# Optimization experiments

Hardware: AMD Instinct MI355X
Metric: run time of the kernel (lower is better)

Reference implementation:

```python
import jax, jax.numpy as jnp
import numpy as np

B = 65536
M = 16          # message_size
DEPTH = 6
WDL = 64
IN_DIM = 45 + 9 * M    # 9 mask + 4*9 board + 9*M messages
OUT_DIM = 9 * M


def setup_inputs() -> dict:
    key = jax.random.key(0)
    ks = jax.random.split(key, 8)
    input_mask = (jax.random.uniform(ks[0], (B, 9, 9)) < 0.5).astype(jnp.float32)
    input_board = (jax.random.uniform(ks[1], (B, 2, 10, 9)) < 0.5).astype(jnp.float32)
    # stacked per-om linears for every depth layer: [depth, 9, in, out]
    layer_w = jax.random.normal(ks[2], (DEPTH, 9, IN_DIM, OUT_DIM), jnp.float32) * (1.0 / np.sqrt(IN_DIM))
    layer_b = jnp.zeros((DEPTH, 9, OUT_DIM), jnp.float32)
    common_w = jax.random.normal(ks[3], (81 * M, 81 + WDL), jnp.float32) * (1.0 / np.sqrt(81 * M))
    common_b = jnp.zeros((81 + WDL,), jnp.float32)
    wdl_w = jax.random.normal(ks[4], (WDL, 3), jnp.float32) * (1.0 / np.sqrt(WDL))
    wdl_b = jnp.zeros((3,), jnp.float32)
    return {
        "input_mask": input_mask,
        "input_board": input_board,
        "layer_w": layer_w,
        "layer_b": layer_b,
        "common_w": common_w,
        "common_b": common_b,
        "wdl_w": wdl_w,
        "wdl_b": wdl_b,
    }


def reference(input_mask, input_board, layer_w, layer_b, common_w, common_b, wdl_w, wdl_b):
    b = input_mask.shape[0]
    m = layer_w.shape[-1] // 9
    depth = layer_w.shape[0]

    # per-om static features: mask[:,om], board[:,0,om], board[:,1,om], global cells
    g0 = jnp.broadcast_to(input_board[:, 0, 9:10, :], (b, 9, 9))
    g1 = jnp.broadcast_to(input_board[:, 1, 9:10, :], (b, 9, 9))
    static = jnp.concatenate(
        [input_mask, input_board[:, 0, :9, :], input_board[:, 1, :9, :], g0, g1],
        axis=-1,
    )  # [B, 9(om), 45]

    messages = jnp.zeros((b, 9, 9, m), input_mask.dtype)  # [B, src_om, dst_om, m]
    for d in range(depth):
        # messages[:, :, om, :] flattened -> gather along axis 2 for each om
        msg_in = messages.transpose(0, 2, 1, 3).reshape(b, 9, 9 * m)  # [B, om, 9m]
        x = jnp.concatenate([static, msg_in], axis=-1)  # [B, 9, 45+9m]
        # 9 distinct small linears, batched as one einsum
        h = jnp.einsum("boi,oij->boj", x, layer_w[d]) + layer_b[d]
        messages = jax.nn.relu(h).reshape(b, 9, 9, m)

    common = messages.reshape(b, 81 * m) @ common_w + common_b
    policy = common[:, :81]
    wdl_hidden = jax.nn.relu(common[:, 81:])
    wdl = wdl_hidden @ wdl_w + wdl_b
    return (wdl, policy)
```

## Files before the change

kernel.cpp:

```cpp
#include <hip/hip_runtime.h>
#include <hip/hip_bf16.h>
#include <stdint.h>


typedef __attribute__((ext_vector_type(4))) float    f32x4;
typedef __attribute__((ext_vector_type(4))) _Float16 f16x4;
typedef __attribute__((ext_vector_type(8))) _Float16 f16x8;
typedef unsigned long long u64;
typedef unsigned int u32;

#define STEP_BYTES 55296
#define PHA_SZ     30720
#define PHB_SZ     24576
#define CMN_STRIDE 41472
#define CSL_SZ     46080
#define CPA_SZ     23040
#define CPB_SZ     18432
#define WS_LAYER   (54*STEP_BYTES)
#define LDS_TOTAL  (2*PHA_SZ)

__device__ __forceinline__ unsigned short f2h(float f) {
  return __builtin_bit_cast(unsigned short, (_Float16)f);
}
__device__ __forceinline__ u64 as_u64(f16x4 v) { return __builtin_bit_cast(u64, v); }
__device__ __forceinline__ f16x4 as_f16x4(u64 v) { return __builtin_bit_cast(f16x4, v); }

__device__ __forceinline__ f32x4 mfma16(f16x4 a, f16x4 b, f32x4 c) {
#if __has_builtin(__builtin_amdgcn_mfma_f32_16x16x16f16)
  return __builtin_amdgcn_mfma_f32_16x16x16f16(a, b, c, 0, 0, 0);
#else
  asm("v_mfma_f32_16x16x16_f16 %0, %1, %2, %0" : "+v"(c) : "v"(a), "v"(b));
  return c;
#endif
}

__device__ __forceinline__ float static_feat(const float* __restrict__ mask,
                                             const float* __restrict__ board,
                                             int b, int o, int kidx) {
  if (kidx < 9)  return mask [b*81  + o*9 + kidx];
  if (kidx < 18) return board[b*180 +       o*9 + (kidx - 9)];
  if (kidx < 27) return board[b*180 + 90 +  o*9 + (kidx - 18)];
  if (kidx < 36) return board[b*180 +       81 + (kidx - 27)];
  if (kidx < 45) return board[b*180 + 90 +  81 + (kidx - 36)];
  return 0.f;
}

template<int NTH>
__device__ __forceinline__ void stage_n(const unsigned char* __restrict__ src,
                                        unsigned char* dstlds, int nbytes, int tid) {
  const int n16 = nbytes / 16;
  const int ubase = tid & ~63;
  for (int k = 0; k * NTH < n16; ++k) {
    const int idx = k * NTH + tid;
    if (idx < n16) {
      __builtin_amdgcn_global_load_lds(
          (const __attribute__((address_space(1))) void*)(src + (size_t)idx * 16),
          (__attribute__((address_space(3))) void*)(dstlds + (size_t)(k * NTH + ubase) * 16),
          16, 0, 0);
    }
  }
}


template<int P, int FIRST>
__device__ __forceinline__ void load_B(u64 (&B)[12],
    const unsigned char* __restrict__ stat, const unsigned char* __restrict__ msg,
    int o, int b0, int s15, int hq, int Bt)
{
  const size_t lo = (size_t)(b0 + s15) * 32 + (size_t)hq * 8;
  B[0] = *(const u64*)(stat + ((size_t)(o * 2 + 0) * Bt) * 32 + lo);
  B[1] = *(const u64*)(stat + ((size_t)(o * 2 + 1) * Bt) * 32 + lo);
  B[2] = *(const u64*)(stat + ((size_t)18 * Bt) * 32 + lo);
  if (!FIRST) {
#pragma unroll
    for (int i = 0; i < 9; ++i) {
      const int cell = P ? (o * 9 + i) : (i * 9 + o);
      B[3 + i] = *(const u64*)(msg + ((size_t)cell * Bt) * 32 + lo);
    }
  }
}

template<int P, int FIRST>
__global__ __launch_bounds__(512, 4) void layer_step(
    const unsigned char* __restrict__ wsLW, const unsigned char* __restrict__ stat,
    unsigned char* __restrict__ msg, int d, int Bt)
{
  __shared__ unsigned char panel[STEP_BYTES];
  const int tid = threadIdx.x;
  const int lane = tid & 63;
  const int wid = tid >> 6;
  const int o = blockIdx.y;
  const int s15 = lane & 15, hq = lane >> 4;

  stage_n<512>(wsLW + (size_t)(d * 9 + o) * STEP_BYTES, panel, STEP_BYTES, tid);

  const int b0 = blockIdx.x * 128 + wid * 16;
  u64 B[12];
  load_B<P, FIRST>(B, stat, msg, o, b0, s15, hq, Bt);

  asm volatile("s_waitcnt vmcnt(0)" ::: "memory");
  __syncthreads();

  const unsigned char* pl = panel + (size_t)lane * 16;
  const size_t lo = (size_t)(b0 + s15) * 32 + (size_t)hq * 8;
#pragma unroll
  for (int j = 0; j < 9; ++j) {
    f32x4 acc = 0.f;
#pragma unroll
    for (int s = 0; s < (FIRST ? 2 : 6); ++s) {
      const f16x8 af = *(const f16x8*)(pl + j * 6144 + s * 1024);
      const f16x4 alo = __builtin_shufflevector(af, af, 0, 1, 2, 3);
      acc = mfma16(alo, as_f16x4(B[2 * s]), acc);
      if (!FIRST || s == 0) {
        const f16x4 ahi = __builtin_shufflevector(af, af, 4, 5, 6, 7);
        acc = mfma16(ahi, as_f16x4(B[2 * s + 1]), acc);
      }
    }
    f16x4 h;
#pragma unroll
    for (int r = 0; r < 4; ++r)
      h[r] = (_Float16)fmaxf(acc[r], 0.f);
    const int wcell = P ? (o * 9 + j) : (j * 9 + o);
    *(u64*)(msg + ((size_t)wcell * Bt) * 32 + lo) = as_u64(h);
  }
}

__global__ __launch_bounds__(256, 4) void common_unf(
    const unsigned char* __restrict__ wsCW, const unsigned char* __restrict__ msg,
    const float* __restrict__ common_b, float* __restrict__ wdlbuf,
    float* __restrict__ out, int Bt)
{
  __shared__ unsigned char sl[CSL_SZ];
  const int tid = threadIdx.x;
  const int lane = tid & 63;
  const int wid = tid >> 6;
  const int s15 = lane & 15, hq = lane >> 4;
  const int b0 = blockIdx.x * 64 + wid * 16;
  const size_t lo = (size_t)(b0 + s15) * 32 + (size_t)hq * 8;

  f32x4 acc[10];
#pragma unroll
  for (int mt = 0; mt < 10; ++mt) acc[mt] = 0.f;

  for (int i = 0; i < 9; ++i) {
    __syncthreads();
    stage_n<256>(wsCW + (size_t)i * CSL_SZ, sl, CSL_SZ, tid);
    asm volatile("s_waitcnt vmcnt(0)" ::: "memory");
    __syncthreads();

    u64 m[9];
#pragma unroll
    for (int jj = 0; jj < 9; ++jj)
      m[jj] = *(const u64*)(msg + ((size_t)(i * 9 + jj) * Bt) * 32 + lo);

#pragma unroll
    for (int mt = 0; mt < 10; ++mt) {
      const unsigned char* base = sl + mt * 4608;
#pragma unroll
      for (int p = 0; p < 4; ++p) {
        const f16x8 a8 = *(const f16x8*)(base + p * 1024 + (size_t)lane * 16);
        const f16x4 alo = __builtin_shufflevector(a8, a8, 0, 1, 2, 3);
        const f16x4 ahi = __builtin_shufflevector(a8, a8, 4, 5, 6, 7);
        acc[mt] = mfma16(alo, as_f16x4(m[2 * p]),     acc[mt]);
        acc[mt] = mfma16(ahi, as_f16x4(m[2 * p + 1]), acc[mt]);
      }
      const f16x4 al = *(const f16x4*)(base + 4096 + (size_t)lane * 8);
      acc[mt] = mfma16(al, as_f16x4(m[8]), acc[mt]);
    }
  }

#pragma unroll
  for (int mt = 0; mt < 10; ++mt) {
#pragma unroll
    for (int r = 0; r < 4; ++r) {
      const int c = mt * 16 + 4 * hq + r;
      if (c < 145) {
        const float v = acc[mt][r] + common_b[c];
        if (c < 81) out[(size_t)3 * Bt + (size_t)(b0 + s15) * 81 + c] = v;
        else        wdlbuf[(size_t)(c - 81) * Bt + (b0 + s15)] = v;
      }
    }
  }
}

__global__ __launch_bounds__(256) void wdl_final(
    const float* __restrict__ wdlbuf, const float* __restrict__ wdl_w,
    const float* __restrict__ wdl_b, float* __restrict__ out, int Bt)
{
  const int b = blockIdx.x * 256 + threadIdx.x;
  if (b >= Bt) return;
  float s0 = wdl_b[0], s1 = wdl_b[1], s2 = wdl_b[2];
  for (int cc = 0; cc < 64; ++cc) {
    const float h = fmaxf(wdlbuf[(size_t)cc * Bt + b], 0.f);
    s0 += h * wdl_w[cc * 3 + 0];
    s1 += h * wdl_w[cc * 3 + 1];
    s2 += h * wdl_w[cc * 3 + 2];
  }
  out[(size_t)b * 3 + 0] = s0;
  out[(size_t)b * 3 + 1] = s1;
  out[(size_t)b * 3 + 2] = s2;
}

__global__ __launch_bounds__(256) void conv_static(
    const float* __restrict__ mask, const float* __restrict__ board,
    unsigned char* __restrict__ stat, int Bt)
{
  const int gid = blockIdx.x * 256 + threadIdx.x;
  if (gid >= 19 * Bt * 4) return;
  const int hq = gid & 3;
  const int b = (gid >> 2) % Bt;
  const int slot = gid / (Bt * 4);
  const int o = (slot < 18) ? (slot >> 1) : 0;
  const int c = (slot < 18) ? (slot & 1) : 2;
  unsigned short v[4];
#pragma unroll
  for (int e = 0; e < 4; ++e) {
    const int kidx = c * 16 + 4 * hq + e;
    v[e] = f2h((kidx == 45) ? 1.f : static_feat(mask, board, b, o, kidx));
  }
  const u32 w0 = (u32)v[0] | ((u32)v[1] << 16);
  const u32 w1 = (u32)v[2] | ((u32)v[3] << 16);
  *(uint2*)(stat + (size_t)gid * 8) = make_uint2(w0, w1);
}

__global__ __launch_bounds__(256) void conv_common_w2(const float* __restrict__ cw,
                                                      unsigned char* __restrict__ dst) {
  const int gid = blockIdx.x * 256 + threadIdx.x;
  const int NPAIR = 10 * 36 * 64;
  if (gid < NPAIR) {
    const int lane = gid & 63;
    const int t = gid >> 6;
    const int p = t % 4, t2 = t / 4;
    const int i = t2 % 9, mt = t2 / 9;
    const int m = lane & 15, hq = lane >> 4;
    const int c = mt * 16 + m;
    unsigned short v[8];
#pragma unroll
    for (int e = 0; e < 8; ++e) {
      const int ci = i * 9 + 2 * p + (e >> 2);
      const int k = ci * 16 + 4 * hq + (e & 3);
      v[e] = f2h((c < 145) ? cw[(size_t)k * 145 + c] : 0.f);
    }
    const u32 w0 = (u32)v[0] | ((u32)v[1] << 16);
    const u32 w1 = (u32)v[2] | ((u32)v[3] << 16);
    const u32 w2 = (u32)v[4] | ((u32)v[5] << 16);
    const u32 w3 = (u32)v[6] | ((u32)v[7] << 16);
    *(uint4*)(dst + (size_t)i * CSL_SZ + (size_t)mt * 4608
              + (size_t)p * 1024 + (size_t)lane * 16) = make_uint4(w0, w1, w2, w3);
  } else if (gid < NPAIR + 10 * 9 * 64) {
    const int g = gid - NPAIR;
    const int lane = g & 63;
    const int t = g >> 6;
    const int i = t % 9, mt = t / 9;
    const int m = lane & 15, hq = lane >> 4;
    const int c = mt * 16 + m;
    unsigned short v[4];
#pragma unroll
    for (int e = 0; e < 4; ++e) {
      const int k = (i * 9 + 8) * 16 + 4 * hq + e;
      v[e] = f2h((c < 145) ? cw[(size_t)k * 145 + c] : 0.f);
    }
    const u32 w0 = (u32)v[0] | ((u32)v[1] << 16);
    const u32 w1 = (u32)v[2] | ((u32)v[3] << 16);
    *(uint2*)(dst + (size_t)i * CSL_SZ + (size_t)mt * 4608
              + 4096 + (size_t)lane * 8) = make_uint2(w0, w1);
  }
}


template<int P, int O, int J0, int J1, int OFF>
__device__ __forceinline__ void jt_range(const unsigned char* __restrict__ buf,
    u64 (&msg)[9][9], const u64 (&msgc)[9], f16x4 st0, f16x4 st1, f16x4 stc, int lane)
{
  const unsigned char* abase = buf + (size_t)lane * 16 - OFF;
#pragma unroll
  for (int j = J0; j < J1; ++j) {
    f32x4 acc = 0.f;
#pragma unroll
    for (int sp = 0; sp < 6; ++sp) {
      const f16x8 af = *(const f16x8*)(abase + j * 6144 + sp * 1024);
      const f16x4 alo = __builtin_shufflevector(af, af, 0, 1, 2, 3);
      const f16x4 ahi = __builtin_shufflevector(af, af, 4, 5, 6, 7);
      const int c0 = 2 * sp, c1 = 2 * sp + 1;
      if (c0 == 0)      acc = mfma16(alo, st0, acc);
      else if (c0 == 2) acc = mfma16(alo, stc, acc);
      else              acc = mfma16(alo, as_f16x4(msgc[c0 - 3]), acc);
      if (c1 == 1)      acc = mfma16(ahi, st1, acc);
      else              acc = mfma16(ahi, as_f16x4(msgc[c1 - 3]), acc);
    }
    f16x4 h;
#pragma unroll
    for (int r = 0; r < 4; ++r)
      h[r] = (_Float16)fmaxf(acc[r], 0.f);
    if (P) msg[O][j] = as_u64(h); else msg[j][O] = as_u64(h);
  }
}

template<int P, int O>
__device__ __forceinline__ void do_step_layer(int base, const unsigned char* __restrict__ ws,
    unsigned char* bufA, unsigned char* bufB, u64 (&msg)[9][9],
    u64 sb, u32 sb8, f16x4 stc, int lane, int tid)
{
  const int step = base + P * 9 + O;
  asm volatile("s_waitcnt vmcnt(0)" ::: "memory");
  __syncthreads();
  stage_n<256>(ws + (size_t)step * STEP_BYTES + PHA_SZ, bufB, PHB_SZ, tid);
  f16x4 st0, st1;
  {
    const u32 byt = (O < 8) ? ((u32)(sb >> (O * 8)) & 0xFFu) : sb8;
#pragma unroll
    for (int e = 0; e < 4; ++e) {
      st0[e] = (_Float16)(float)((byt >> e) & 1u);
      st1[e] = (_Float16)(float)((byt >> (4 + e)) & 1u);
    }
  }
  u64 msgc[9];
#pragma unroll
  for (int i = 0; i < 9; ++i)
    msgc[i] = P ? msg[O][i] : msg[i][O];
  jt_range<P, O, 0, 5, 0>(bufA, msg, msgc, st0, st1, stc, lane);
  asm volatile("s_waitcnt vmcnt(0)" ::: "memory");
  __syncthreads();
  if (step + 1 < 54)
    stage_n<256>(ws + (size_t)(step + 1) * STEP_BYTES, bufA, PHA_SZ, tid);
  else
    stage_n<256>(ws + WS_LAYER, bufA, CPA_SZ, tid);
  jt_range<P, O, 5, 9, PHA_SZ>(bufB, msg, msgc, st0, st1, stc, lane);
}

__global__ __launch_bounds__(256, 1) void mix_main(
    const float* __restrict__ mask, const float* __restrict__ board,
    const float* __restrict__ common_b, const float* __restrict__ wdl_w,
    const float* __restrict__ wdl_b, const unsigned char* __restrict__ ws,
    float* __restrict__ out, int Bt)
{
  extern __shared__ unsigned char lds[];
  const int tid = threadIdx.x;
  const int lane = tid & 63;
  const int wid = tid >> 6;
  const int s15 = lane & 15, hq = lane >> 4;
  const int b0 = blockIdx.x * 64 + wid * 16;
  unsigned char* bufA = lds;
  unsigned char* bufB = lds + PHA_SZ;

  stage_n<256>(ws, bufA, PHA_SZ, tid);

  u64 msg[9][9];
#pragma unroll
  for (int a = 0; a < 9; ++a)
#pragma unroll
    for (int b = 0; b < 9; ++b) msg[a][b] = 0ull;

  u64 sb = 0ull;
  u32 sb8 = 0u;
  {
    const int b = b0 + s15;
#pragma unroll
    for (int o = 0; o < 9; ++o)
#pragma unroll
      for (int e = 0; e < 4; ++e) {
        const u32 bit0 = static_feat(mask, board, b, o,      4 * hq + e) > 0.5f;
        const u32 bit1 = static_feat(mask, board, b, o, 16 + 4 * hq + e) > 0.5f;
        if (o < 8) sb |= ((u64)bit0 << (o * 8 + e)) | ((u64)bit1 << (o * 8 + 4 + e));
        else       sb8 |= (bit0 << e) | (bit1 << (4 + e));
      }
  }
  f16x4 stc;
  {
    const int b = b0 + s15;
#pragma unroll
    for (int e = 0; e < 4; ++e) {
      const int kidx = 32 + 4 * hq + e;
      stc[e] = (_Float16)((kidx == 45) ? 1.f : static_feat(mask, board, b, 0, kidx));
    }
  }

#define DO_POS(P, O) do_step_layer<P, O>(base, ws, bufA, bufB, msg, sb, sb8, stc, lane, tid);
  for (int dp = 0; dp < 3; ++dp) {
    const int base = dp * 18;
    DO_POS(0,0) DO_POS(0,1) DO_POS(0,2) DO_POS(0,3) DO_POS(0,4)
    DO_POS(0,5) DO_POS(0,6) DO_POS(0,7) DO_POS(0,8)
    DO_POS(1,0) DO_POS(1,1) DO_POS(1,2) DO_POS(1,3) DO_POS(1,4)
    DO_POS(1,5) DO_POS(1,6) DO_POS(1,7) DO_POS(1,8)
  }
#undef DO_POS

  float pw[3] = {0.f, 0.f, 0.f};
  for (int mt = 0; mt < 10; ++mt) {
    asm volatile("s_waitcnt vmcnt(0)" ::: "memory");
    __syncthreads();
    stage_n<256>(ws + WS_LAYER + (size_t)mt * CMN_STRIDE + CPA_SZ, bufB, CPB_SZ, tid);
    f32x4 a0 = 0.f;
#pragma unroll
    for (int i = 0; i < 5; ++i) {
      const unsigned char* base = bufA + i * 4608;
#pragma unroll
      for (int p = 0; p < 4; ++p) {
        const f16x8 af = *(const f16x8*)(base + p * 1024 + (size_t)lane * 16);
        const f16x4 alo = __builtin_shufflevector(af, af, 0, 1, 2, 3);
        const f16x4 ahi = __builtin_shufflevector(af, af, 4, 5, 6, 7);
        a0 = mfma16(alo, as_f16x4(msg[i][2 * p]),     a0);
        a0 = mfma16(ahi, as_f16x4(msg[i][2 * p + 1]), a0);
      }
      const f16x4 al = *(const f16x4*)(base + 4096 + (size_t)lane * 8);
      a0 = mfma16(al, as_f16x4(msg[i][8]), a0);
    }
    asm volatile("s_waitcnt vmcnt(0)" ::: "memory");
    __syncthreads();
    if (mt + 1 < 10)
      stage_n<256>(ws + WS_LAYER + (size_t)(mt + 1) * CMN_STRIDE, bufA, CPA_SZ, tid);
#pragma unroll
    for (int i = 5; i < 9; ++i) {
      const unsigned char* base = bufB + i * 4608 - CPA_SZ;
#pragma unroll
      for (int p = 0; p < 4; ++p) {
        const f16x8 af = *(const f16x8*)(base + p * 1024 + (size_t)lane * 16);
        const f16x4 alo = __builtin_shufflevector(af, af, 0, 1, 2, 3);
        const f16x4 ahi = __builtin_shufflevector(af, af, 4, 5, 6, 7);
        a0 = mfma16(alo, as_f16x4(msg[i][2 * p]),     a0);
        a0 = mfma16(ahi, as_f16x4(msg[i][2 * p + 1]), a0);
      }
      const f16x4 al = *(const f16x4*)(base + 4096 + (size_t)lane * 8);
      a0 = mfma16(al, as_f16x4(msg[i][8]), a0);
    }
#pragma unroll
    for (int r = 0; r < 4; ++r) {
      const int c = mt * 16 + 4 * hq + r;
      const float bias = (c < 145) ? common_b[c] : 0.f;
      const float v0 = a0[r] + bias;
      if (c < 81) {
        out[(size_t)3 * Bt + (size_t)(b0 + s15) * 81 + c] = v0;
      } else if (c < 145) {
        const float h0 = fmaxf(v0, 0.f);
        const int cc = c - 81;
#pragma unroll
        for (int w = 0; w < 3; ++w)
          pw[w] += h0 * wdl_w[cc * 3 + w];
      }
    }
  }
#pragma unroll
  for (int w = 0; w < 3; ++w) {
    float v0 = pw[w];
    v0 += __shfl_xor(v0, 16, 64); v0 += __shfl_xor(v0, 32, 64);
    if (hq == 0)
      out[(size_t)(b0 + s15) * 3 + w] = v0 + wdl_b[w];
  }
}


__global__ __launch_bounds__(256) void conv_layer_w(const float* __restrict__ lw,
                                                    const float* __restrict__ lb,
                                                    unsigned char* __restrict__ dst) {
  const int gid = blockIdx.x * 256 + threadIdx.x;
  if (gid >= 54 * 9 * 6 * 64) return;
  const int lane = gid & 63;
  const int t = gid >> 6;
  const int kp = t % 6, t2 = t / 6;
  const int jp = t2 % 9, dop = t2 / 9;
  const int m = lane & 15, hq = lane >> 4;
  unsigned short v[8];
#pragma unroll
  for (int e = 0; e < 8; ++e) {
    const int kc = kp * 2 + (e >> 2);
    const int kidx = kc * 16 + 4 * hq + (e & 3);
    float f = 0.f;
    if (kidx < 45)        f = lw[((size_t)dop * 189 + kidx) * 144 + jp * 16 + m];
    else if (kidx == 45)  f = lb[(size_t)dop * 144 + jp * 16 + m];
    else if (kidx >= 48)  f = lw[((size_t)dop * 189 + (kidx - 3)) * 144 + jp * 16 + m];
    v[e] = f2h(f);
  }
  const u32 w0 = (u32)v[0] | ((u32)v[1] << 16);
  const u32 w1 = (u32)v[2] | ((u32)v[3] << 16);
  const u32 w2 = (u32)v[4] | ((u32)v[5] << 16);
  const u32 w3 = (u32)v[6] | ((u32)v[7] << 16);
  *(uint4*)(dst + (size_t)gid * 16) = make_uint4(w0, w1, w2, w3);
}

__global__ __launch_bounds__(256) void conv_common_w(const float* __restrict__ cw,
                                                     unsigned char* __restrict__ dst) {
  const int gid = blockIdx.x * 256 + threadIdx.x;
  const int NPAIR = 10 * 36 * 64;
  if (gid < NPAIR) {
    const int lane = gid & 63;
    const int t = gid >> 6;
    const int p = t % 4, t2 = t / 4;
    const int i = t2 % 9, mt = t2 / 9;
    const int m = lane & 15, hq = lane >> 4;
    const int c = mt * 16 + m;
    unsigned short v[8];
#pragma unroll
    for (int e = 0; e < 8; ++e) {
      const int ci = i * 9 + 2 * p + (e >> 2);
      const int k = ci * 16 + 4 * hq + (e & 3);
      v[e] = f2h((c < 145) ? cw[(size_t)k * 145 + c] : 0.f);
    }
    const u32 w0 = (u32)v[0] | ((u32)v[1] << 16);
    const u32 w1 = (u32)v[2] | ((u32)v[3] << 16);
    const u32 w2 = (u32)v[4] | ((u32)v[5] << 16);
    const u32 w3 = (u32)v[6] | ((u32)v[7] << 16);
    *(uint4*)(dst + (size_t)WS_LAYER + (size_t)mt * CMN_STRIDE + (size_t)i * 4608
              + (size_t)p * 1024 + (size_t)lane * 16) = make_uint4(w0, w1, w2, w3);
  } else if (gid < NPAIR + 10 * 9 * 64) {
    const int g = gid - NPAIR;
    const int lane = g & 63;
    const int t = g >> 6;
    const int i = t % 9, mt = t / 9;
    const int m = lane & 15, hq = lane >> 4;
    const int c = mt * 16 + m;
    unsigned short v[4];
#pragma unroll
    for (int e = 0; e < 4; ++e) {
      const int k = (i * 9 + 8) * 16 + 4 * hq + e;
      v[e] = f2h((c < 145) ? cw[(size_t)k * 145 + c] : 0.f);
    }
    const u32 w0 = (u32)v[0] | ((u32)v[1] << 16);
    const u32 w1 = (u32)v[2] | ((u32)v[3] << 16);
    *(uint2*)(dst + (size_t)WS_LAYER + (size_t)mt * CMN_STRIDE + (size_t)i * 4608
              + 4096 + (size_t)lane * 8) = make_uint2(w0, w1);
  }
}


extern "C" void kernel_launch(void* const* d_in, const int* in_sizes, int n_in,
                              void* d_out, int out_size, void* d_ws, size_t ws_size,
                              hipStream_t stream) {
  const float* mask     = (const float*)d_in[0];
  const float* board    = (const float*)d_in[1];
  const float* layer_w  = (const float*)d_in[2];
  const float* layer_b  = (const float*)d_in[3];
  const float* common_w = (const float*)d_in[4];
  const float* common_b = (const float*)d_in[5];
  const float* wdl_w    = (const float*)d_in[6];
  const float* wdl_b    = (const float*)d_in[7];
  float* out = (float*)d_out;
  unsigned char* ws = (unsigned char*)d_ws;
  const int Bt = in_sizes[0] / 81;

  const size_t WS_CW_OFF   = (size_t)WS_LAYER;
  const size_t WS_STAT_OFF = WS_CW_OFF + (size_t)9 * CSL_SZ;
  const size_t WS_MSG_OFF  = WS_STAT_OFF + (size_t)19 * Bt * 32;
  const size_t WS_WDL_OFF  = WS_MSG_OFF + (size_t)81 * Bt * 32;
  const size_t WS_NEED     = WS_WDL_OFF + (size_t)64 * Bt * 4;

  hipLaunchKernelGGL(conv_layer_w, dim3((54 * 9 * 6 * 64) / 256), dim3(256), 0, stream,
                     layer_w, layer_b, ws);

  if (ws_size >= WS_NEED) {
    unsigned char* stat = ws + WS_STAT_OFF;
    unsigned char* msgp = ws + WS_MSG_OFF;
    float* wdlbuf = (float*)(ws + WS_WDL_OFF);

    hipLaunchKernelGGL(conv_common_w2, dim3((10 * (36 + 9) * 64 + 255) / 256), dim3(256),
                       0, stream, common_w, ws + WS_CW_OFF);
    hipLaunchKernelGGL(conv_static, dim3((19 * Bt * 4 + 255) / 256), dim3(256), 0, stream,
                       mask, board, stat, Bt);

    const dim3 lgrid(Bt / 128, 9);
    hipLaunchKernelGGL((layer_step<0, 1>), lgrid, dim3(512), 0, stream, ws, stat, msgp, 0, Bt);
    hipLaunchKernelGGL((layer_step<1, 0>), lgrid, dim3(512), 0, stream, ws, stat, msgp, 1, Bt);
    hipLaunchKernelGGL((layer_step<0, 0>), lgrid, dim3(512), 0, stream, ws, stat, msgp, 2, Bt);
    hipLaunchKernelGGL((layer_step<1, 0>), lgrid, dim3(512), 0, stream, ws, stat, msgp, 3, Bt);
    hipLaunchKernelGGL((layer_step<0, 0>), lgrid, dim3(512), 0, stream, ws, stat, msgp, 4, Bt);
    hipLaunchKernelGGL((layer_step<1, 0>), lgrid, dim3(512), 0, stream, ws, stat, msgp, 5, Bt);

    hipLaunchKernelGGL(common_unf, dim3(Bt / 64), dim3(256), 0, stream,
                       ws + WS_CW_OFF, msgp, common_b, wdlbuf, out, Bt);
    hipLaunchKernelGGL(wdl_final, dim3((Bt + 255) / 256), dim3(256), 0, stream,
                       wdlbuf, wdl_w, wdl_b, out, Bt);
  } else {
    hipLaunchKernelGGL(conv_common_w, dim3((10 * (36 + 9) * 64 + 255) / 256), dim3(256),
                       0, stream, common_w, ws);
    (void)hipFuncSetAttribute((const void*)mix_main,
                              hipFuncAttributeMaxDynamicSharedMemorySize, LDS_TOTAL);
    hipLaunchKernelGGL(mix_main, dim3(Bt / 64), dim3(256), LDS_TOTAL, stream,
                       mask, board, common_b, wdl_w, wdl_b, ws, out, Bt);
  }
}
```

Before: 533.9 us.

## Double per-wave batch tile, fuse WDL head into common kernel, stage static via LDS

Each wave in layer_step and common_unf now handles two 16-row batch tiles, so every LDS weight fragment feeds twice as many MFMAs and the per-layer panel staging is amortized over 256 rows instead of 128. The WDL hidden ReLU and 64x3 projection move into common_unf epilogue with cross-lane shuffles, removing the wdlbuf round trip and the wdl_final launch. conv_static now loads mask/board tiles into shared memory with coalesced float4 reads before packing to fp16. The cost is higher register pressure (common_unf launch bound lowered to 3) and half as many blocks per launch, which may reduce occupancy; message loads in common_unf are also issued before the LDS wait to overlap with staging.

```diff
diff --git a/kernel.cpp b/kernel.cpp
--- a/kernel.cpp
+++ b/kernel.cpp
@@ -94,64 +94,76 @@
 
   stage_n<512>(wsLW + (size_t)(d * 9 + o) * STEP_BYTES, panel, STEP_BYTES, tid);
 
-  const int b0 = blockIdx.x * 128 + wid * 16;
-  u64 B[12];
-  load_B<P, FIRST>(B, stat, msg, o, b0, s15, hq, Bt);
+  const int b0 = blockIdx.x * 256 + wid * 32;
+  u64 B0[12], B1[12];
+  load_B<P, FIRST>(B0, stat, msg, o, b0,      s15, hq, Bt);
+  load_B<P, FIRST>(B1, stat, msg, o, b0 + 16, s15, hq, Bt);
 
   asm volatile("s_waitcnt vmcnt(0)" ::: "memory");
   __syncthreads();
 
   const unsigned char* pl = panel + (size_t)lane * 16;
-  const size_t lo = (size_t)(b0 + s15) * 32 + (size_t)hq * 8;
+  const size_t lo0 = (size_t)(b0 + s15) * 32 + (size_t)hq * 8;
+  const size_t lo1 = lo0 + 16 * 32;
 #pragma unroll
   for (int j = 0; j < 9; ++j) {
-    f32x4 acc = 0.f;
+    f32x4 a0 = 0.f, a1 = 0.f;
 #pragma unroll
     for (int s = 0; s < (FIRST ? 2 : 6); ++s) {
       const f16x8 af = *(const f16x8*)(pl + j * 6144 + s * 1024);
       const f16x4 alo = __builtin_shufflevector(af, af, 0, 1, 2, 3);
-      acc = mfma16(alo, as_f16x4(B[2 * s]), acc);
+      a0 = mfma16(alo, as_f16x4(B0[2 * s]), a0);
+      a1 = mfma16(alo, as_f16x4(B1[2 * s]), a1);
       if (!FIRST || s == 0) {
         const f16x4 ahi = __builtin_shufflevector(af, af, 4, 5, 6, 7);
-        acc = mfma16(ahi, as_f16x4(B[2 * s + 1]), acc);
+        a0 = mfma16(ahi, as_f16x4(B0[2 * s + 1]), a0);
+        a1 = mfma16(ahi, as_f16x4(B1[2 * s + 1]), a1);
       }
     }
-    f16x4 h;
-#pragma unroll
-    for (int r = 0; r < 4; ++r)
-      h[r] = (_Float16)fmaxf(acc[r], 0.f);
+    f16x4 h0, h1;
+#pragma unroll
+    for (int r = 0; r < 4; ++r) {
+      h0[r] = (_Float16)fmaxf(a0[r], 0.f);
+      h1[r] = (_Float16)fmaxf(a1[r], 0.f);
+    }
     const int wcell = P ? (o * 9 + j) : (j * 9 + o);
-    *(u64*)(msg + ((size_t)wcell * Bt) * 32 + lo) = as_u64(h);
-  }
-}
-
-__global__ __launch_bounds__(256, 4) void common_unf(
+    unsigned char* wp = msg + ((size_t)wcell * Bt) * 32;
+    *(u64*)(wp + lo0) = as_u64(h0);
+    *(u64*)(wp + lo1) = as_u64(h1);
+  }
+}
+
+__global__ __launch_bounds__(256, 3) void common_unf(
     const unsigned char* __restrict__ wsCW, const unsigned char* __restrict__ msg,
-    const float* __restrict__ common_b, float* __restrict__ wdlbuf,
-    float* __restrict__ out, int Bt)
+    const float* __restrict__ common_b, const float* __restrict__ wdl_w,
+    const float* __restrict__ wdl_b, float* __restrict__ out, int Bt)
 {
   __shared__ unsigned char sl[CSL_SZ];
   const int tid = threadIdx.x;
   const int lane = tid & 63;
   const int wid = tid >> 6;
   const int s15 = lane & 15, hq = lane >> 4;
-  const int b0 = blockIdx.x * 64 + wid * 16;
-  const size_t lo = (size_t)(b0 + s15) * 32 + (size_t)hq * 8;
-
-  f32x4 acc[10];
-#pragma unroll
-  for (int mt = 0; mt < 10; ++mt) acc[mt] = 0.f;
+  const int b0 = blockIdx.x * 128 + wid * 32;
+  const size_t lo0 = (size_t)(b0 + s15) * 32 + (size_t)hq * 8;
+  const size_t lo1 = lo0 + 16 * 32;
+
+  f32x4 acc0[10], acc1[10];
+#pragma unroll
+  for (int mt = 0; mt < 10; ++mt) { acc0[mt] = 0.f; acc1[mt] = 0.f; }
 
   for (int i = 0; i < 9; ++i) {
     __syncthreads();
     stage_n<256>(wsCW + (size_t)i * CSL_SZ, sl, CSL_SZ, tid);
+
+    u64 m0[9], m1[9];
+#pragma unroll
+    for (int jj = 0; jj < 9; ++jj) {
+      const unsigned char* mp = msg + ((size_t)(i * 9 + jj) * Bt) * 32;
+      m0[jj] = *(const u64*)(mp + lo0);
+      m1[jj] = *(const u64*)(mp + lo1);
+    }
     asm volatile("s_waitcnt vmcnt(0)" ::: "memory");
     __syncthreads();
-
-    u64 m[9];
-#pragma unroll
-    for (int jj = 0; jj < 9; ++jj)
-      m[jj] = *(const u64*)(msg + ((size_t)(i * 9 + jj) * Bt) * 32 + lo);
 
 #pragma unroll
     for (int mt = 0; mt < 10; ++mt) {
@@ -161,66 +173,92 @@
         const f16x8 a8 = *(const f16x8*)(base + p * 1024 + (size_t)lane * 16);
         const f16x4 alo = __builtin_shufflevector(a8, a8, 0, 1, 2, 3);
         const f16x4 ahi = __builtin_shufflevector(a8, a8, 4, 5, 6, 7);
-        acc[mt] = mfma16(alo, as_f16x4(m[2 * p]),     acc[mt]);
-        acc[mt] = mfma16(ahi, as_f16x4(m[2 * p + 1]), acc[mt]);
+        acc0[mt] = mfma16(alo, as_f16x4(m0[2 * p]),     acc0[mt]);
+        acc1[mt] = mfma16(alo, as_f16x4(m1[2 * p]),     acc1[mt]);
+        acc0[mt] = mfma16(ahi, as_f16x4(m0[2 * p + 1]), acc0[mt]);
+        acc1[mt] = mfma16(ahi, as_f16x4(m1[2 * p + 1]), acc1[mt]);
       }
       const f16x4 al = *(const f16x4*)(base + 4096 + (size_t)lane * 8);
-      acc[mt] = mfma16(al, as_f16x4(m[8]), acc[mt]);
-    }
-  }
-
+      acc0[mt] = mfma16(al, as_f16x4(m0[8]), acc0[mt]);
+      acc1[mt] = mfma16(al, as_f16x4(m1[8]), acc1[mt]);
+    }
+  }
+
+  float pw0[3] = {0.f, 0.f, 0.f}, pw1[3] = {0.f, 0.f, 0.f};
 #pragma unroll
   for (int mt = 0; mt < 10; ++mt) {
 #pragma unroll
     for (int r = 0; r < 4; ++r) {
       const int c = mt * 16 + 4 * hq + r;
-      if (c < 145) {
-        const float v = acc[mt][r] + common_b[c];
-        if (c < 81) out[(size_t)3 * Bt + (size_t)(b0 + s15) * 81 + c] = v;
-        else        wdlbuf[(size_t)(c - 81) * Bt + (b0 + s15)] = v;
+      if (c < 81) {
+        out[(size_t)3 * Bt + (size_t)(b0 + s15) * 81 + c]      = acc0[mt][r] + common_b[c];
+        out[(size_t)3 * Bt + (size_t)(b0 + 16 + s15) * 81 + c] = acc1[mt][r] + common_b[c];
+      } else if (c < 145) {
+        const float h0 = fmaxf(acc0[mt][r] + common_b[c], 0.f);
+        const float h1 = fmaxf(acc1[mt][r] + common_b[c], 0.f);
+        const int cc = c - 81;
+#pragma unroll
+        for (int w = 0; w < 3; ++w) {
+          const float wv = wdl_w[cc * 3 + w];
+          pw0[w] += h0 * wv;
+          pw1[w] += h1 * wv;
+        }
       }
     }
   }
-}
-
-__global__ __launch_bounds__(256) void wdl_final(
-    const float* __restrict__ wdlbuf, const float* __restrict__ wdl_w,
-    const float* __restrict__ wdl_b, float* __restrict__ out, int Bt)
-{
-  const int b = blockIdx.x * 256 + threadIdx.x;
-  if (b >= Bt) return;
-  float s0 = wdl_b[0], s1 = wdl_b[1], s2 = wdl_b[2];
-  for (int cc = 0; cc < 64; ++cc) {
-    const float h = fmaxf(wdlbuf[(size_t)cc * Bt + b], 0.f);
-    s0 += h * wdl_w[cc * 3 + 0];
-    s1 += h * wdl_w[cc * 3 + 1];
-    s2 += h * wdl_w[cc * 3 + 2];
-  }
-  out[(size_t)b * 3 + 0] = s0;
-  out[(size_t)b * 3 + 1] = s1;
-  out[(size_t)b * 3 + 2] = s2;
+#pragma unroll
+  for (int w = 0; w < 3; ++w) {
+    float v0 = pw0[w], v1 = pw1[w];
+    v0 += __shfl_xor(v0, 16, 64); v0 += __shfl_xor(v0, 32, 64);
+    v1 += __shfl_xor(v1, 16, 64); v1 += __shfl_xor(v1, 32, 64);
+    if (hq == 0) {
+      const float bb = wdl_b[w];
+      out[(size_t)(b0 + s15) * 3 + w]      = v0 + bb;
+      out[(size_t)(b0 + 16 + s15) * 3 + w] = v1 + bb;
+    }
+  }
 }
 
 __global__ __launch_bounds__(256) void conv_static(
     const float* __restrict__ mask, const float* __restrict__ board,
     unsigned char* __restrict__ stat, int Bt)
 {
-  const int gid = blockIdx.x * 256 + threadIdx.x;
-  if (gid >= 19 * Bt * 4) return;
-  const int hq = gid & 3;
-  const int b = (gid >> 2) % Bt;
-  const int slot = gid / (Bt * 4);
-  const int o = (slot < 18) ? (slot >> 1) : 0;
-  const int c = (slot < 18) ? (slot & 1) : 2;
-  unsigned short v[4];
-#pragma unroll
-  for (int e = 0; e < 4; ++e) {
-    const int kidx = c * 16 + 4 * hq + e;
-    v[e] = f2h((kidx == 45) ? 1.f : static_feat(mask, board, b, o, kidx));
-  }
-  const u32 w0 = (u32)v[0] | ((u32)v[1] << 16);
-  const u32 w1 = (u32)v[2] | ((u32)v[3] << 16);
-  *(uint2*)(stat + (size_t)gid * 8) = make_uint2(w0, w1);
+  __shared__ float sm[16 * 81];
+  __shared__ float sb[16 * 180];
+  const int tid = threadIdx.x;
+  const int base_b = blockIdx.x * 16;
+
+  const float4* gm = (const float4*)(mask + (size_t)base_b * 81);
+  for (int idx = tid; idx < 324; idx += 256) ((float4*)sm)[idx] = gm[idx];
+  const float4* gb = (const float4*)(board + (size_t)base_b * 180);
+  for (int idx = tid; idx < 720; idx += 256) ((float4*)sb)[idx] = gb[idx];
+  __syncthreads();
+
+  const int lane = tid & 63, wv = tid >> 6;
+  const int s15 = lane & 15, hq = lane >> 4;
+  const float* lm = sm + s15 * 81;
+  const float* lb = sb + s15 * 180;
+  for (int slot = wv; slot < 19; slot += 4) {
+    const int o = (slot < 18) ? (slot >> 1) : 0;
+    const int c = (slot < 18) ? (slot & 1) : 2;
+    unsigned short v[4];
+#pragma unroll
+    for (int e = 0; e < 4; ++e) {
+      const int kidx = c * 16 + 4 * hq + e;
+      float f;
+      if (kidx < 9)        f = lm[o * 9 + kidx];
+      else if (kidx < 18)  f = lb[o * 9 + (kidx - 9)];
+      else if (kidx < 27)  f = lb[90 + o * 9 + (kidx - 18)];
+      else if (kidx < 36)  f = lb[81 + (kidx - 27)];
+      else if (kidx < 45)  f = lb[90 + 81 + (kidx - 36)];
+      else                 f = (kidx == 45) ? 1.f : 0.f;
+      v[e] = f2h(f);
+    }
+    const u32 w0 = (u32)v[0] | ((u32)v[1] << 16);
+    const u32 w1 = (u32)v[2] | ((u32)v[3] << 16);
+    *(uint2*)(stat + ((size_t)slot * Bt + base_b + s15) * 32 + (size_t)hq * 8)
+        = make_uint2(w0, w1);
+  }
 }
 
 __global__ __launch_bounds__(256) void conv_common_w2(const float* __restrict__ cw,
@@ -402,7 +440,7 @@
         a0 = mfma16(alo, as_f16x4(msg[i][2 * p]),     a0);
         a0 = mfma16(ahi, as_f16x4(msg[i][2 * p + 1]), a0);
       }
-      const f16x4 al = *(const f16x4*)(base + 4096 + (size_t)lane * 8);
+      const f16x4 al = *(const f16x4*)(bufA + i * 4608 + 4096 + (size_t)lane * 8);
       a0 = mfma16(al, as_f16x4(msg[i][8]), a0);
     }
     asm volatile("s_waitcnt vmcnt(0)" ::: "memory");
@@ -540,8 +578,7 @@
   const size_t WS_CW_OFF   = (size_t)WS_LAYER;
   const size_t WS_STAT_OFF = WS_CW_OFF + (size_t)9 * CSL_SZ;
   const size_t WS_MSG_OFF  = WS_STAT_OFF + (size_t)19 * Bt * 32;
-  const size_t WS_WDL_OFF  = WS_MSG_OFF + (size_t)81 * Bt * 32;
-  const size_t WS_NEED     = WS_WDL_OFF + (size_t)64 * Bt * 4;
+  const size_t WS_NEED     = WS_MSG_OFF + (size_t)81 * Bt * 32;
 
   hipLaunchKernelGGL(conv_layer_w, dim3((54 * 9 * 6 * 64) / 256), dim3(256), 0, stream,
                      layer_w, layer_b, ws);
@@ -549,14 +586,13 @@
   if (ws_size >= WS_NEED) {
     unsigned char* stat = ws + WS_STAT_OFF;
     unsigned char* msgp = ws + WS_MSG_OFF;
-    float* wdlbuf = (float*)(ws + WS_WDL_OFF);
 
     hipLaunchKernelGGL(conv_common_w2, dim3((10 * (36 + 9) * 64 + 255) / 256), dim3(256),
                        0, stream, common_w, ws + WS_CW_OFF);
-    hipLaunchKernelGGL(conv_static, dim3((19 * Bt * 4 + 255) / 256), dim3(256), 0, stream,
+    hipLaunchKernelGGL(conv_static, dim3(Bt / 16), dim3(256), 0, stream,
                        mask, board, stat, Bt);
 
-    const dim3 lgrid(Bt / 128, 9);
+    const dim3 lgrid(Bt / 256, 9);
     hipLaunchKernelGGL((layer_step<0, 1>), lgrid, dim3(512), 0, stream, ws, stat, msgp, 0, Bt);
     hipLaunchKernelGGL((layer_step<1, 0>), lgrid, dim3(512), 0, stream, ws, stat, msgp, 1, Bt);
     hipLaunchKernelGGL((layer_step<0, 0>), lgrid, dim3(512), 0, stream, ws, stat, msgp, 2, Bt);
@@ -564,10 +600,8 @@
     hipLaunchKernelGGL((layer_step<0, 0>), lgrid, dim3(512), 0, stream, ws, stat, msgp, 4, Bt);
     hipLaunchKernelGGL((layer_step<1, 0>), lgrid, dim3(512), 0, stream, ws, stat, msgp, 5, Bt);
 
-    hipLaunchKernelGGL(common_unf, dim3(Bt / 64), dim3(256), 0, stream,
-                       ws + WS_CW_OFF, msgp, common_b, wdlbuf, out, Bt);
-    hipLaunchKernelGGL(wdl_final, dim3((Bt + 255) / 256), dim3(256), 0, stream,
-                       wdlbuf, wdl_w, wdl_b, out, Bt);
+    hipLaunchKernelGGL(common_unf, dim3(Bt / 128), dim3(256), 0, stream,
+                       ws + WS_CW_OFF, msgp, common_b, wdl_w, wdl_b, out, Bt);
   } else {
     hipLaunchKernelGGL(conv_common_w, dim3((10 * (36 + 9) * 64 + 255) / 256), dim3(256),
                        0, stream, common_w, ws);
```

After: 451.7 us. 1.18x faster.
